# Performance work log

Measured on AMD Instinct MI355X. Metric: run time of the kernel, lower is better.

Reference implementation:

```python
import jax, jax.numpy as jnp
import numpy as np

D_MODEL = 256
D_STATE = 64
D_CONV = 4
EXPAND = 2
HEADDIM = 16
D_INNER = EXPAND * D_MODEL            # 512
NHEADS = D_INNER // HEADDIM           # 32
CONV_DIM = D_INNER + 2 * D_STATE      # 640 (ngroups=1)
D_IN_PROJ = 2 * D_INNER + 2 * D_STATE + NHEADS  # 1184
BATCH = 256
SEQ = 200


def _ln(x, g, b, eps=1e-12):
    m = jnp.mean(x, axis=-1, keepdims=True)
    v = jnp.mean((x - m) ** 2, axis=-1, keepdims=True)
    return (x - m) * jax.lax.rsqrt(v + eps) * g + b


def setup_inputs() -> dict:
    key = jax.random.key(0)
    ks = jax.random.split(key, 16)
    def gn(i, shape, s=0.02):
        return jax.random.normal(ks[i], shape, jnp.float32) * s
    return {
        "input_tensor": jax.random.normal(ks[0], (BATCH, SEQ, D_MODEL), jnp.float32),
        # Mamba2 params
        "in_proj_w": gn(1, (D_MODEL, D_IN_PROJ)),
        "conv_w": gn(2, (CONV_DIM, D_CONV), 0.1),
        "conv_b": jnp.zeros((CONV_DIM,), jnp.float32),
        "dt_bias": gn(3, (NHEADS,), 0.1),
        "A_log": jnp.log(jax.random.uniform(ks[4], (NHEADS,), jnp.float32, 1.0, 16.0)),
        "D_skip": jnp.ones((NHEADS,), jnp.float32),
        "rms_w": jnp.ones((D_INNER,), jnp.float32),
        "out_proj_w": gn(5, (D_INNER, D_MODEL)),
        # Layer norms / mixers
        "ln_g": jnp.ones((D_MODEL,), jnp.float32),
        "ln_b": jnp.zeros((D_MODEL,), jnp.float32),
        "filt_w": gn(6, (1, SEQ // 2 + 1, D_MODEL, 2), 0.02),
        "filt_ln_g": jnp.ones((D_MODEL,), jnp.float32),
        "filt_ln_b": jnp.zeros((D_MODEL,), jnp.float32),
        "alpha": jax.random.uniform(ks[7], (D_MODEL,), jnp.float32),
        "beta": jax.random.uniform(ks[8], (D_MODEL,), jnp.float32),
        # FFN
        "ffn_w1": gn(9, (D_MODEL, 4 * D_MODEL)),
        "ffn_b1": jnp.zeros((4 * D_MODEL,), jnp.float32),
        "ffn_w2": gn(10, (4 * D_MODEL, D_MODEL)),
        "ffn_b2": jnp.zeros((D_MODEL,), jnp.float32),
        "ffn_ln_g": jnp.ones((D_MODEL,), jnp.float32),
        "ffn_ln_b": jnp.zeros((D_MODEL,), jnp.float32),
    }


def _mamba2(x, in_proj_w, conv_w, conv_b, dt_bias, A_log, D_skip, rms_w, out_proj_w):
    b, l, _ = x.shape
    zxbcdt = x @ in_proj_w                                  # [b,l,1184]
    z, xBC, dt = jnp.split(zxbcdt, [D_INNER, D_INNER + CONV_DIM], axis=-1)
    # depthwise causal conv over time + SiLU
    xp = jnp.pad(xBC, ((0, 0), (D_CONV - 1, 0), (0, 0)))
    conv = conv_b + sum(conv_w[:, k] * xp[:, k:k + l, :] for k in range(D_CONV))
    xBC = jax.nn.silu(conv)
    xs, Bm, Cm = jnp.split(xBC, [D_INNER, D_INNER + D_STATE], axis=-1)
    xh = xs.reshape(b, l, NHEADS, HEADDIM)
    dt = jax.nn.softplus(dt + dt_bias)                      # [b,l,h]
    A = -jnp.exp(A_log)                                     # [h]
    dA = jnp.exp(dt * A)                                    # [b,l,h]
    dtx = dt[..., None] * xh                                # [b,l,h,p]

    def step(state, inp):
        dA_t, dtx_t, B_t, C_t = inp
        # state: [b,h,p,n]
        state = dA_t[:, :, None, None] * state + dtx_t[..., None] * B_t[:, None, None, :]
        y_t = jnp.einsum('bhpn,bn->bhp', state, C_t)
        return state, y_t

    state0 = jnp.zeros((b, NHEADS, HEADDIM, D_STATE), x.dtype)
    _, y = jax.lax.scan(step, state0,
                        (jnp.moveaxis(dA, 1, 0), jnp.moveaxis(dtx, 1, 0),
                         jnp.moveaxis(Bm, 1, 0), jnp.moveaxis(Cm, 1, 0)))
    y = jnp.moveaxis(y, 0, 1) + D_skip[None, None, :, None] * xh   # skip connection
    y = y.reshape(b, l, D_INNER)
    # gated RMSNorm: rmsnorm(y * silu(z)) * w
    g = y * jax.nn.silu(z)
    g = g * jax.lax.rsqrt(jnp.mean(g * g, axis=-1, keepdims=True) + 1e-5) * rms_w
    return g @ out_proj_w


def reference(input_tensor, in_proj_w, conv_w, conv_b, dt_bias, A_log, D_skip,
              rms_w, out_proj_w, ln_g, ln_b, filt_w, filt_ln_g, filt_ln_b,
              alpha, beta, ffn_w1, ffn_b1, ffn_w2, ffn_b2, ffn_ln_g, ffn_ln_b):
    x = input_tensor
    h1 = _mamba2(x, in_proj_w, conv_w, conv_b, dt_bias, A_log, D_skip, rms_w, out_proj_w)
    h1 = _ln(h1 + x, ln_g, ln_b)
    # FFT filter branch
    xf = jnp.fft.rfft(x, axis=1, norm='ortho')
    w = filt_w[..., 0] + 1j * filt_w[..., 1]                # [1,101,d]
    xi = jnp.fft.irfft(xf * w, n=SEQ, axis=1, norm='ortho').astype(x.dtype)
    h2 = _ln(xi + x, filt_ln_g, filt_ln_b)
    h = alpha * h1 + beta * h2
    hid = jax.nn.gelu(h @ ffn_w1 + ffn_b1, approximate=False) @ ffn_w2 + ffn_b2
    return _ln(hid + h, ffn_ln_g, ffn_ln_b)
```

## Files before the change

kernel.cpp:

```cpp
#include <hip/hip_runtime.h>
#include <math.h>

#define BATCHN 256
#define SEQ 200
#define DMODEL 256
#define DINNER 512
#define NH 32
#define HD 16
#define DSTATE 64
#define DINPROJ 1184
#define XBCLD 672
#define BL (BATCHN*SEQ)
#define NF 101
#define XBASE 655360
#define TC 20
#define NCH 10
#define XIOFF 8500000

typedef __attribute__((ext_vector_type(8))) short bf16x8;
typedef __attribute__((ext_vector_type(4))) float f32x4;

__device__ inline unsigned short f2bf(float f) {
    union { float f; unsigned u; } v; v.f = f;
    unsigned r = v.u + 0x7FFFu + ((v.u >> 16) & 1u);
    return (unsigned short)(r >> 16);
}
__device__ inline float bf2f(unsigned short h) {
    union { unsigned u; float f; } v; v.u = ((unsigned)h) << 16;
    return v.f;
}

#define GLOAD16(src, dst) __builtin_amdgcn_global_load_lds( \
    (const __attribute__((address_space(1))) void*)(src),   \
    (__attribute__((address_space(3))) void*)(dst), 16, 0, 0)

__global__ void init_dft_kernel(unsigned short* __restrict__ EF, unsigned short* __restrict__ EI)
{
    const float ang = 6.28318530717958647692f / 200.0f;
    int idx = blockIdx.x * 256 + threadIdx.x;
    if (idx < 256 * SEQ) {
        int f = idx / SEQ, t = idx - f * SEQ;
        float v;
        if (f <= 100) { int ph = (f * t) % 200; v = cosf(ang * (float)ph); }
        else if (f <= 201) { int ff = f - 101; int ph = (ff * t) % 200; v = -sinf(ang * (float)ph); }
        else v = 0.f;
        EF[idx] = f2bf(v);
    } else if (idx < 256 * SEQ + 256 * 256) {
        int j2 = idx - 256 * SEQ;
        int t = j2 >> 8, j = j2 & 255;
        float v;
        if (t >= 200) v = 0.f;
        else if (j == 0) v = 1.0f / 200.0f;
        else if (j == 100) v = ((t & 1) ? -1.0f : 1.0f) / 200.0f;
        else if (j < 100) { int ph = (j * t) % 200; v = 2.0f * cosf(ang * (float)ph) / 200.0f; }
        else if (j >= 202 || j == 101 || j == 201) v = 0.0f;
        else { int f = j - 101; int ph = (f * t) % 200; v = -2.0f * sinf(ang * (float)ph) / 200.0f; }
        EI[j2] = f2bf(v);
    }
}

#define S0 303104
#define S1 131072
#define S2 262144
#define S3 262144
#define S4 1638400
__global__ void setup_kernel(const float* __restrict__ ipw, const float* __restrict__ opw,
                             const float* __restrict__ w1, const float* __restrict__ w2,
                             const float* __restrict__ X,
                             unsigned short* __restrict__ wTall, unsigned short* __restrict__ opwT,
                             unsigned short* __restrict__ w1T, unsigned short* __restrict__ w2T,
                             unsigned short* __restrict__ xbf)
{
    long long idx = (long long)blockIdx.x * 256 + threadIdx.x;
    if (idx < S0) { int n = (int)(idx / 256), k = (int)(idx % 256);
        wTall[idx] = f2bf(ipw[(long long)k * DINPROJ + n]); return; }
    idx -= S0;
    if (idx < S1) { int n = (int)(idx / 512), k = (int)(idx % 512);
        opwT[idx] = f2bf(opw[(long long)k * 256 + n]); return; }
    idx -= S1;
    if (idx < S2) { int n = (int)(idx / 256), k = (int)(idx % 256);
        w1T[idx] = f2bf(w1[(long long)k * 1024 + n]); return; }
    idx -= S2;
    if (idx < S3) { int n = (int)(idx / 1024), k = (int)(idx % 1024);
        w2T[idx] = f2bf(w2[(long long)k * 256 + n]); return; }
    idx -= S3;
    if (idx < S4) {
        long long i = idx * 8;
        float4 a = ((const float4*)(X + i))[0];
        float4 b = ((const float4*)(X + i))[1];
        uint4 o;
        o.x = (unsigned)f2bf(a.x) | ((unsigned)f2bf(a.y) << 16);
        o.y = (unsigned)f2bf(a.z) | ((unsigned)f2bf(a.w) << 16);
        o.z = (unsigned)f2bf(b.x) | ((unsigned)f2bf(b.y) << 16);
        o.w = (unsigned)f2bf(b.z) | ((unsigned)f2bf(b.w) << 16);
        *(uint4*)(xbf + i) = o;
    }
}

__global__ void xT_kernel(const float* __restrict__ X, unsigned short* __restrict__ XT)
{
    __shared__ float tile[32][33];
    int b = blockIdx.z, t0 = blockIdx.x * 32, d0 = blockIdx.y * 32;
    int tx = threadIdx.x & 31, ty = threadIdx.x >> 5;
    const float* xb = X + (long long)b * SEQ * DMODEL;
#pragma unroll
    for (int i = 0; i < 4; i++) {
        int t = t0 + ty + i * 8;
        tile[ty + i * 8][tx] = (t < SEQ) ? xb[(long long)t * DMODEL + d0 + tx] : 0.f;
    }
    __syncthreads();
    unsigned short* xtb = XT + (long long)b * DMODEL * SEQ;
#pragma unroll
    for (int i = 0; i < 4; i++) {
        int d = d0 + ty + i * 8;
        int t = t0 + tx;
        if (t < SEQ) xtb[(long long)d * SEQ + t] = f2bf(tile[tx][ty + i * 8]);
    }
}

template<int ACT, int CBF>
__global__ __launch_bounds__(256) void mgemm_kernel(
    const unsigned short* __restrict__ Ab, const unsigned short* __restrict__ BTp,
    void* __restrict__ Cp, const float* __restrict__ bias,
    int M, int N, int K, int lda, int ldbt, int ldc,
    long long sA, long long sBT, long long sC)
{
    __shared__ unsigned short As[128 * 32];
    __shared__ unsigned short Bs[128 * 32];
    const unsigned short* Aa = Ab + (long long)blockIdx.z * sA;
    const unsigned short* Bt = BTp + (long long)blockIdx.z * sBT;
    float* Cf = (float*)Cp + (CBF ? 0 : (long long)blockIdx.z * sC);
    unsigned short* Cb = (unsigned short*)Cp + (CBF ? (long long)blockIdx.z * sC : 0);

    int m0 = blockIdx.y * 128, n0 = blockIdx.x * 128;
    int tid = threadIdx.x;
    int srow = tid >> 1, skb = (tid & 1) * 16;
    int w = tid >> 6, l = tid & 63;
    int wr = w >> 1, wc = w & 1;
    int fr = l & 15, fk = l >> 4;
    int glr = (w << 4) + (l >> 2);
    int glc = (l & 3) << 3;
    bool fullM = (m0 + 128 <= M);
    bool fullN = (n0 + 128 <= N);

    f32x4 acc[4][4] = {};

    for (int k0 = 0; k0 < K; k0 += 32) {
        bool kedge = (k0 + 32 > K);
        if (fullM && !kedge) {
            GLOAD16(Aa + (long long)(m0 + glr) * lda + k0 + glc,      &As[w << 9]);
            GLOAD16(Aa + (long long)(m0 + 64 + glr) * lda + k0 + glc, &As[2048 + (w << 9)]);
        } else {
            int gm = m0 + srow;
            unsigned short* dst = &As[srow * 32 + skb];
#pragma unroll
            for (int i = 0; i < 16; i++) {
                int gk = k0 + skb + i;
                dst[i] = (gm < M && gk < K) ? Aa[(long long)gm * lda + gk] : (unsigned short)0;
            }
        }
        if (fullN && !kedge) {
            GLOAD16(Bt + (long long)(n0 + glr) * ldbt + k0 + glc,      &Bs[w << 9]);
            GLOAD16(Bt + (long long)(n0 + 64 + glr) * ldbt + k0 + glc, &Bs[2048 + (w << 9)]);
        } else {
            int gn = n0 + srow;
            unsigned short* dst = &Bs[srow * 32 + skb];
#pragma unroll
            for (int i = 0; i < 16; i++) {
                int gk = k0 + skb + i;
                dst[i] = (gn < N && gk < K) ? Bt[(long long)gn * ldbt + gk] : (unsigned short)0;
            }
        }
        __syncthreads();
        bf16x8 a[4], b[4];
#pragma unroll
        for (int i = 0; i < 4; i++) {
            a[i] = *(const bf16x8*)&As[(wr * 64 + i * 16 + fr) * 32 + fk * 8];
            b[i] = *(const bf16x8*)&Bs[(wc * 64 + i * 16 + fr) * 32 + fk * 8];
        }
#pragma unroll
        for (int i = 0; i < 4; i++)
#pragma unroll
            for (int j = 0; j < 4; j++)
                acc[i][j] = __builtin_amdgcn_mfma_f32_16x16x32_bf16(a[i], b[j], acc[i][j], 0, 0, 0);
        __syncthreads();
    }

#pragma unroll
    for (int i = 0; i < 4; i++) {
        int gr0 = m0 + wr * 64 + i * 16 + fk * 4;
#pragma unroll
        for (int j = 0; j < 4; j++) {
            int gc = n0 + wc * 64 + j * 16 + fr;
            if (gc >= N) continue;
            float bv = bias ? bias[gc] : 0.f;
#pragma unroll
            for (int r = 0; r < 4; r++) {
                int gr = gr0 + r;
                if (gr >= M) continue;
                float v = acc[i][j][r] + bv;
                if (ACT == 1) v = 0.5f * v * (1.f + erff(v * 0.70710678118654752f));
                long long ci = (long long)gr * ldc + gc;
                if (CBF) Cb[ci] = f2bf(v);
                else Cf[ci] = v;
            }
        }
    }
}

__global__ __launch_bounds__(256) void mgemm_proj(
    const unsigned short* __restrict__ Aa, const unsigned short* __restrict__ Bt,
    float* __restrict__ XBCout, unsigned short* __restrict__ Zout)
{
    __shared__ unsigned short As[128 * 32];
    __shared__ unsigned short Bs[128 * 32];
    const int N = DINPROJ;
    int m0 = blockIdx.y * 128, n0 = blockIdx.x * 128;
    int tid = threadIdx.x;
    int srow = tid >> 1, skb = (tid & 1) * 16;
    int w = tid >> 6, l = tid & 63;
    int wr = w >> 1, wc = w & 1;
    int fr = l & 15, fk = l >> 4;
    int glr = (w << 4) + (l >> 2);
    int glc = (l & 3) << 3;
    bool fullN = (n0 + 128 <= N);

    f32x4 acc[4][4] = {};

    for (int k0 = 0; k0 < 256; k0 += 32) {
        GLOAD16(Aa + (long long)(m0 + glr) * 256 + k0 + glc,      &As[w << 9]);
        GLOAD16(Aa + (long long)(m0 + 64 + glr) * 256 + k0 + glc, &As[2048 + (w << 9)]);
        if (fullN) {
            GLOAD16(Bt + (long long)(n0 + glr) * 256 + k0 + glc,      &Bs[w << 9]);
            GLOAD16(Bt + (long long)(n0 + 64 + glr) * 256 + k0 + glc, &Bs[2048 + (w << 9)]);
        } else {
            int gn = n0 + srow;
            unsigned short* dst = &Bs[srow * 32 + skb];
#pragma unroll
            for (int i = 0; i < 16; i++)
                dst[i] = (gn < N) ? Bt[(long long)gn * 256 + k0 + skb + i] : (unsigned short)0;
        }
        __syncthreads();
        bf16x8 a[4], b[4];
#pragma unroll
        for (int i = 0; i < 4; i++) {
            a[i] = *(const bf16x8*)&As[(wr * 64 + i * 16 + fr) * 32 + fk * 8];
            b[i] = *(const bf16x8*)&Bs[(wc * 64 + i * 16 + fr) * 32 + fk * 8];
        }
#pragma unroll
        for (int i = 0; i < 4; i++)
#pragma unroll
            for (int j = 0; j < 4; j++)
                acc[i][j] = __builtin_amdgcn_mfma_f32_16x16x32_bf16(a[i], b[j], acc[i][j], 0, 0, 0);
        __syncthreads();
    }

#pragma unroll
    for (int i = 0; i < 4; i++) {
        int gr0 = m0 + wr * 64 + i * 16 + fk * 4;
#pragma unroll
        for (int j = 0; j < 4; j++) {
            int gc = n0 + wc * 64 + j * 16 + fr;
            if (gc >= N) continue;
#pragma unroll
            for (int r = 0; r < 4; r++) {
                int gr = gr0 + r;
                float v = acc[i][j][r];
                if (gc < 512) Zout[(long long)gr * 512 + gc] = f2bf(v);
                else XBCout[(long long)gr * XBCLD + (gc - 512)] = v;
            }
        }
    }
}

__global__ void convbc_kernel(const float* __restrict__ XBC, const float* __restrict__ conv_w,
                              const float* __restrict__ conv_b, const float* __restrict__ dt_bias,
                              const float* __restrict__ A_log,
                              float* __restrict__ BCb, float* __restrict__ DTb, float* __restrict__ DAb,
                              float* __restrict__ BCF)
{
    __shared__ float sB[64];
    int row = blockIdx.x;
    int b = row / SEQ, l = row - b * SEQ;
    int tid = threadIdx.x;
    float v = 0.f;
    if (tid < 128) {
        int ch = 512 + tid;
        float acc = conv_b[ch];
#pragma unroll
        for (int k = 0; k < 4; k++) {
            int lt = l + k - 3;
            if (lt >= 0)
                acc = fmaf(conv_w[ch * 4 + k], XBC[(long long)(b * SEQ + lt) * XBCLD + ch], acc);
        }
        v = acc * __builtin_amdgcn_rcpf(1.f + __expf(-acc));
        BCb[(long long)row * 128 + tid] = v;
        if (tid < 64) sB[tid] = v;
    } else if (tid < 160) {
        int h = tid - 128;
        float draw = XBC[(long long)row * XBCLD + 640 + h] + dt_bias[h];
        float dtv = (draw > 20.f) ? draw : log1pf(__expf(draw));
        DTb[(long long)row * NH + h] = dtv;
        DAb[(long long)row * NH + h] = __expf(-__expf(A_log[h]) * dtv);
    }
    __syncthreads();
    if (tid >= 64 && tid < 128) {
        int n = tid - 64;
        float prod = sB[n] * v;
#pragma unroll
        for (int m = 1; m < 64; m <<= 1) prod += __shfl_xor(prod, m);
        if (n == 0) BCF[row] = prod;
    }
}

__device__ __forceinline__ void sstep2(
    float raw, float dtv, float da, float bc,
    const float4& qb0, const float4& qb1, const float4& qb2, const float4& qb3,
    const float4& qc0, const float4& qc1, const float4& qc2, const float4& qc3,
    float cw0, float cw1, float cw2, float cw3, float cb, float ds,
    float* st, float& w0, float& w1, float& w2,
    int lane, float* __restrict__ yaddr)
{
    float cvv = cb + cw0 * w0 + cw1 * w1 + cw2 * w2 + cw3 * raw;
    float xhv = cvv * __builtin_amdgcn_rcpf(1.f + __expf(-cvv));
    w0 = w1; w1 = w2; w2 = raw;
    float xv = dtv * xhv;
    float p0 = st[0]  * qc0.x;
    float p1 = st[1]  * qc0.y;
    float p2 = st[2]  * qc0.z;
    float p3 = st[3]  * qc0.w;
    p0 = fmaf(st[4],  qc1.x, p0);
    p1 = fmaf(st[5],  qc1.y, p1);
    p2 = fmaf(st[6],  qc1.z, p2);
    p3 = fmaf(st[7],  qc1.w, p3);
    p0 = fmaf(st[8],  qc2.x, p0);
    p1 = fmaf(st[9],  qc2.y, p1);
    p2 = fmaf(st[10], qc2.z, p2);
    p3 = fmaf(st[11], qc2.w, p3);
    p0 = fmaf(st[12], qc3.x, p0);
    p1 = fmaf(st[13], qc3.y, p1);
    p2 = fmaf(st[14], qc3.z, p2);
    p3 = fmaf(st[15], qc3.w, p3);
    st[0]  = fmaf(da, st[0],  xv * qb0.x);
    st[1]  = fmaf(da, st[1],  xv * qb0.y);
    st[2]  = fmaf(da, st[2],  xv * qb0.z);
    st[3]  = fmaf(da, st[3],  xv * qb0.w);
    st[4]  = fmaf(da, st[4],  xv * qb1.x);
    st[5]  = fmaf(da, st[5],  xv * qb1.y);
    st[6]  = fmaf(da, st[6],  xv * qb1.z);
    st[7]  = fmaf(da, st[7],  xv * qb1.w);
    st[8]  = fmaf(da, st[8],  xv * qb2.x);
    st[9]  = fmaf(da, st[9],  xv * qb2.y);
    st[10] = fmaf(da, st[10], xv * qb2.z);
    st[11] = fmaf(da, st[11], xv * qb2.w);
    st[12] = fmaf(da, st[12], xv * qb3.x);
    st[13] = fmaf(da, st[13], xv * qb3.y);
    st[14] = fmaf(da, st[14], xv * qb3.z);
    st[15] = fmaf(da, st[15], xv * qb3.w);
    float part = (p0 + p1) + (p2 + p3);
    part += __shfl_xor(part, 16);
    part += __shfl_xor(part, 32);
    if (lane < HD) *yaddr = fmaf(da, part, fmaf(xv, bc, ds * xhv));
}

__global__ __launch_bounds__(256) void scan7b_kernel(
    const float* __restrict__ DTb, const float* __restrict__ DAb,
    float* __restrict__ XBC, const float* __restrict__ BCb,
    const float* __restrict__ Dsk,
    const float* __restrict__ conv_w, const float* __restrict__ conv_b,
    const float* __restrict__ BCF)
{
    __shared__ float sbc[2][TC][128];
    __shared__ unsigned short sx[2][TC][128];
    __shared__ float sdt[2][TC][8];
    __shared__ float sda[2][TC][8];
    __shared__ float sbcf[2][TC];
    int tid = threadIdx.x;
    int wv = tid >> 6, lane = tid & 63;
    int bid = blockIdx.x;
    int b = bid >> 2, hq = (bid & 3) * 8;
    long long rowb = (long long)b * SEQ;

    for (int i = tid; i < TC * 32; i += 256) {
        int r = i >> 5, c = i & 31;
        ((float4*)&sbc[0][r][0])[c] = ((const float4*)(BCb + (rowb + r) * 128))[c];
    }
    for (int i = tid; i < TC * 64; i += 256) {
        int r = i >> 6, c2 = i & 63;
        float2 v = *(const float2*)(XBC + (rowb + r) * XBCLD + hq * 16 + (c2 << 1));
        *(unsigned*)&sx[0][r][c2 << 1] = (unsigned)f2bf(v.x) | ((unsigned)f2bf(v.y) << 16);
    }
    for (int i = tid; i < TC * 8; i += 256) {
        int t = i >> 3, j = i & 7;
        sdt[0][t][j] = DTb[(rowb + t) * NH + hq + j];
        sda[0][t][j] = DAb[(rowb + t) * NH + hq + j];
    }
    if (tid < TC) sbcf[0][tid] = BCF[rowb + tid];
    __syncthreads();

    int p = lane & 15, g = lane >> 4;
    int hA = hq + wv, hB = hq + 4 + wv;
    int chA = hA * HD + p, chB = hB * HD + p;
    float cwA0 = conv_w[chA * 4 + 0], cwA1 = conv_w[chA * 4 + 1];
    float cwA2 = conv_w[chA * 4 + 2], cwA3 = conv_w[chA * 4 + 3];
    float cbA = conv_b[chA];
    float cwB0 = conv_w[chB * 4 + 0], cwB1 = conv_w[chB * 4 + 1];
    float cwB2 = conv_w[chB * 4 + 2], cwB3 = conv_w[chB * 4 + 3];
    float cbB = conv_b[chB];
    float dsA = Dsk[hA], dsB = Dsk[hB];
    int xcA = wv * 16 + p, xcB = (4 + wv) * 16 + p;
    float* ypA = XBC + rowb * XBCLD + hA * HD + p;
    float* ypB = XBC + rowb * XBCLD + hB * HD + p;
    float stA[16], stB[16];
#pragma unroll
    for (int r = 0; r < 16; r++) { stA[r] = 0.f; stB[r] = 0.f; }
    float wA0 = 0.f, wA1 = 0.f, wA2 = 0.f;
    float wB0 = 0.f, wB1 = 0.f, wB2 = 0.f;

    for (int c = 0; c < NCH; c++) {
        int cur = c & 1;
        if (c + 1 < NCH) {
            int nb = cur ^ 1;
            long long tb = rowb + (c + 1) * TC;
            for (int i = tid; i < TC * 32; i += 256) {
                int r = i >> 5, cc = i & 31;
                ((float4*)&sbc[nb][r][0])[cc] = ((const float4*)(BCb + (tb + r) * 128))[cc];
            }
            for (int i = tid; i < TC * 64; i += 256) {
                int r = i >> 6, c2 = i & 63;
                float2 v = *(const float2*)(XBC + (tb + r) * XBCLD + hq * 16 + (c2 << 1));
                *(unsigned*)&sx[nb][r][c2 << 1] = (unsigned)f2bf(v.x) | ((unsigned)f2bf(v.y) << 16);
            }
            for (int i = tid; i < TC * 8; i += 256) {
                int t = i >> 3, j = i & 7;
                sdt[nb][t][j] = DTb[(tb + t) * NH + hq + j];
                sda[nb][t][j] = DAb[(tb + t) * NH + hq + j];
            }
            if (tid < TC) sbcf[nb][tid] = BCF[tb + tid];
        }
        int tbase = c * TC;
        for (int t = 0; t < TC; t++) {
            int gt = tbase + t;
            const float4* qb = (const float4*)&sbc[cur][t][g * 16];
            const float4* qc = (const float4*)&sbc[cur][t][64 + g * 16];
            float4 qb0 = qb[0], qb1 = qb[1], qb2 = qb[2], qb3 = qb[3];
            float4 qc0 = qc[0], qc1 = qc[1], qc2 = qc[2], qc3 = qc[3];
            float rawA = bf2f(sx[cur][t][xcA]);
            float rawB = bf2f(sx[cur][t][xcB]);
            float bc = sbcf[cur][t];
            sstep2(rawA, sdt[cur][t][wv], sda[cur][t][wv], bc,
                   qb0, qb1, qb2, qb3, qc0, qc1, qc2, qc3,
                   cwA0, cwA1, cwA2, cwA3, cbA, dsA, stA, wA0, wA1, wA2,
                   lane, ypA + (long long)gt * XBCLD);
            sstep2(rawB, sdt[cur][t][4 + wv], sda[cur][t][4 + wv], bc,
                   qb0, qb1, qb2, qb3, qc0, qc1, qc2, qc3,
                   cwB0, cwB1, cwB2, cwB3, cbB, dsB, stB, wB0, wB1, wB2,
                   lane, ypB + (long long)gt * XBCLD);
        }
        __syncthreads();
    }
}

__global__ __launch_bounds__(256) void gate_kernel(
    float* __restrict__ XBC, const unsigned short* __restrict__ Zbf,
    const float* __restrict__ rms_w)
{
    int row = blockIdx.x * 4 + (threadIdx.x >> 6);
    int lane = threadIdx.x & 63;
    float* yrow = XBC + (long long)row * XBCLD + lane * 8;
    const unsigned short* zrow = Zbf + (long long)row * 512 + lane * 8;
    float4 y0 = ((const float4*)yrow)[0];
    float4 y1 = ((const float4*)yrow)[1];
    uint4 zq = ((const uint4*)zrow)[0];
    float yv[8] = { y0.x, y0.y, y0.z, y0.w, y1.x, y1.y, y1.z, y1.w };
    float zv[8];
    zv[0] = bf2f((unsigned short)(zq.x & 0xFFFF)); zv[1] = bf2f((unsigned short)(zq.x >> 16));
    zv[2] = bf2f((unsigned short)(zq.y & 0xFFFF)); zv[3] = bf2f((unsigned short)(zq.y >> 16));
    zv[4] = bf2f((unsigned short)(zq.z & 0xFFFF)); zv[5] = bf2f((unsigned short)(zq.z >> 16));
    zv[6] = bf2f((unsigned short)(zq.w & 0xFFFF)); zv[7] = bf2f((unsigned short)(zq.w >> 16));
    float a[8]; float ss = 0.f;
#pragma unroll
    for (int i = 0; i < 8; i++) {
        float z = zv[i];
        a[i] = yv[i] * (z * __builtin_amdgcn_rcpf(1.f + __expf(-z)));
        ss = fmaf(a[i], a[i], ss);
    }
#pragma unroll
    for (int m = 1; m < 64; m <<= 1) ss += __shfl_xor(ss, m);
    float sc = rsqrtf(ss * (1.f / 512.f) + 1e-5f);
    const float* rw = rms_w + lane * 8;
    float4 r0 = ((const float4*)rw)[0];
    float4 r1 = ((const float4*)rw)[1];
    float rv[8] = { r0.x, r0.y, r0.z, r0.w, r1.x, r1.y, r1.z, r1.w };
    uint4 o;
    o.x = (unsigned)f2bf(a[0] * sc * rv[0]) | ((unsigned)f2bf(a[1] * sc * rv[1]) << 16);
    o.y = (unsigned)f2bf(a[2] * sc * rv[2]) | ((unsigned)f2bf(a[3] * sc * rv[3]) << 16);
    o.z = (unsigned)f2bf(a[4] * sc * rv[4]) | ((unsigned)f2bf(a[5] * sc * rv[5]) << 16);
    o.w = (unsigned)f2bf(a[6] * sc * rv[6]) | ((unsigned)f2bf(a[7] * sc * rv[7]) << 16);
    unsigned short* grow = (unsigned short*)(XBC + (long long)row * XBCLD);
    ((uint4*)grow)[lane] = o;
}

__global__ void lnadd_bf_kernel(const unsigned short* __restrict__ A, const float* __restrict__ Bb,
                                const float* __restrict__ g, const float* __restrict__ be,
                                float* __restrict__ O)
{
    int row = blockIdx.x * 4 + (threadIdx.x >> 6);
    int lane = threadIdx.x & 63;
    long long base = (long long)row * DMODEL + lane * 4;
    float v[4]; float s1 = 0.f;
#pragma unroll
    for (int i = 0; i < 4; i++) { float a = bf2f(A[base + i]) + Bb[base + i]; v[i] = a; s1 += a; }
#pragma unroll
    for (int m = 1; m < 64; m <<= 1) s1 += __shfl_xor(s1, m);
    float mean = s1 * (1.f / 256.f);
    float s2 = 0.f;
#pragma unroll
    for (int i = 0; i < 4; i++) { float d = v[i] - mean; s2 = fmaf(d, d, s2); }
#pragma unroll
    for (int m = 1; m < 64; m <<= 1) s2 += __shfl_xor(s2, m);
    float r = rsqrtf(s2 * (1.f / 256.f) + 1e-12f);
#pragma unroll
    for (int i = 0; i < 4; i++)
        O[base + i] = (v[i] - mean) * r * g[lane * 4 + i] + be[lane * 4 + i];
}

__global__ void combine2_kernel(const float* __restrict__ XI, const float* __restrict__ X,
                                float* __restrict__ MO, unsigned short* __restrict__ HB,
                                const float* __restrict__ lg, const float* __restrict__ lb,
                                const float* __restrict__ fg, const float* __restrict__ fb,
                                const float* __restrict__ al, const float* __restrict__ bt)
{
    int row = blockIdx.x * 4 + (threadIdx.x >> 6);
    int lane = threadIdx.x & 63;
    long long base = (long long)row * DMODEL + lane * 4;
    int bb = row / SEQ, ll = row - bb * SEQ;
    long long xib = (long long)bb * 65536 + ll * 256 + lane * 4;
    float u[4], v[4]; float su = 0.f, sv = 0.f;
#pragma unroll
    for (int i = 0; i < 4; i++) {
        float xv = X[base + i];
        float a = MO[base + i] + xv;
        float b = XI[xib + i] + xv;
        u[i] = a; v[i] = b; su += a; sv += b;
    }
#pragma unroll
    for (int m = 1; m < 64; m <<= 1) { su += __shfl_xor(su, m); sv += __shfl_xor(sv, m); }
    float mu = su * (1.f / 256.f), mv = sv * (1.f / 256.f);
    float qu = 0.f, qv = 0.f;
#pragma unroll
    for (int i = 0; i < 4; i++) {
        float du = u[i] - mu; qu = fmaf(du, du, qu);
        float dv = v[i] - mv; qv = fmaf(dv, dv, qv);
    }
#pragma unroll
    for (int m = 1; m < 64; m <<= 1) { qu += __shfl_xor(qu, m); qv += __shfl_xor(qv, m); }
    float ru = rsqrtf(qu * (1.f / 256.f) + 1e-12f);
    float rv = rsqrtf(qv * (1.f / 256.f) + 1e-12f);
#pragma unroll
    for (int i = 0; i < 4; i++) {
        int d = lane * 4 + i;
        float h1 = (u[i] - mu) * ru * lg[d] + lb[d];
        float h2 = (v[i] - mv) * rv * fg[d] + fb[d];
        float h = al[d] * h1 + bt[d] * h2;
        MO[base + i] = h;
        HB[base + i] = f2bf(h);
    }
}

__global__ void filt_kernel(unsigned short* __restrict__ XF, const float* __restrict__ W)
{
    long long idx = (long long)blockIdx.x * 256 + threadIdx.x;
    if (idx >= (long long)BATCHN * DMODEL * NF) return;
    int f = (int)(idx % NF);
    int d = (int)((idx / NF) % DMODEL);
    int b = (int)(idx / ((long long)NF * DMODEL));
    long long base = ((long long)b * DMODEL + d) * 256;
    float re = bf2f(XF[base + f]);
    float im = bf2f(XF[base + 101 + f]);
    float wr = W[((long long)f * DMODEL + d) * 2];
    float wi = W[((long long)f * DMODEL + d) * 2 + 1];
    XF[base + f]       = f2bf(re * wr - im * wi);
    XF[base + 101 + f] = f2bf(re * wi + im * wr);
}

extern "C" void kernel_launch(void* const* d_in, const int* in_sizes, int n_in,
                              void* d_out, int out_size, void* d_ws, size_t ws_size,
                              hipStream_t stream)
{
    const float* x          = (const float*)d_in[0];
    const float* in_proj_w  = (const float*)d_in[1];
    const float* conv_w     = (const float*)d_in[2];
    const float* conv_b     = (const float*)d_in[3];
    const float* dt_bias    = (const float*)d_in[4];
    const float* A_log      = (const float*)d_in[5];
    const float* D_skip     = (const float*)d_in[6];
    const float* rms_w      = (const float*)d_in[7];
    const float* out_proj_w = (const float*)d_in[8];
    const float* ln_g       = (const float*)d_in[9];
    const float* ln_b       = (const float*)d_in[10];
    const float* filt_w     = (const float*)d_in[11];
    const float* filt_ln_g  = (const float*)d_in[12];
    const float* filt_ln_b  = (const float*)d_in[13];
    const float* alpha      = (const float*)d_in[14];
    const float* beta       = (const float*)d_in[15];
    const float* ffn_w1     = (const float*)d_in[16];
    const float* ffn_b1     = (const float*)d_in[17];
    const float* ffn_w2     = (const float*)d_in[18];
    const float* ffn_b2     = (const float*)d_in[19];
    const float* ffn_ln_g   = (const float*)d_in[20];
    const float* ffn_ln_b   = (const float*)d_in[21];
    float* out = (float*)d_out;
    float* ws = (float*)d_ws;

    unsigned short* WP    = (unsigned short*)(ws + 81920);
    unsigned short* wTall = WP;
    unsigned short* opwT  = wTall + 1184 * 256;
    unsigned short* w1T   = opwT + 256 * 512;
    unsigned short* w2T   = w1T + 1024 * 256;
    unsigned short* EFbf  = w2T + 256 * 1024;
    unsigned short* EIbf  = EFbf + 256 * SEQ;
    float* XBC = ws + XBASE;
    float* BCb = XBC + (long long)BL * XBCLD;
    float* DTb = BCb + (long long)BL * 128;
    float* DAb = DTb + (long long)BL * NH;
    float* MO  = DAb + (long long)BL * NH;
    float* BCF = MO + (long long)BL * DMODEL;
    unsigned short* Zbf = (unsigned short*)MO;
    unsigned short* xbf  = (unsigned short*)BCb;
    unsigned short* xTbf = (unsigned short*)BCb;
    unsigned short* MObf = (unsigned short*)BCb;
    unsigned short* Gbf = (unsigned short*)XBC;
    unsigned short* XFT = (unsigned short*)XBC;
    float* XI  = XBC + XIOFF;
    unsigned short* HID = (unsigned short*)XBC;
    unsigned short* FFO = (unsigned short*)(XBC + 26500000);

    init_dft_kernel<<<dim3((256 * SEQ + 256 * 256 + 255) / 256), dim3(256), 0, stream>>>(EFbf, EIbf);
    setup_kernel<<<dim3((S0 + S1 + S2 + S3 + S4) / 256), dim3(256), 0, stream>>>(
        in_proj_w, out_proj_w, ffn_w1, ffn_w2, x, wTall, opwT, w1T, w2T, xbf);

    mgemm_proj<<<dim3(10, BL / 128), dim3(256), 0, stream>>>(xbf, wTall, XBC, Zbf);

    convbc_kernel<<<dim3(BL), dim3(192), 0, stream>>>(XBC, conv_w, conv_b, dt_bias, A_log,
                                                      BCb, DTb, DAb, BCF);

    scan7b_kernel<<<dim3(BATCHN * 4), dim3(256), 0, stream>>>(DTb, DAb, XBC, BCb, D_skip,
                                                              conv_w, conv_b, BCF);

    xT_kernel<<<dim3(7, 8, BATCHN), dim3(256), 0, stream>>>(x, xTbf);

    gate_kernel<<<dim3(BL / 4), dim3(256), 0, stream>>>(XBC, Zbf, rms_w);

    mgemm_kernel<0,0><<<dim3(2, BL / 128, 1), dim3(256), 0, stream>>>(
        Gbf, opwT, MO, nullptr, BL, 256, 512, 1344, 512, 256, 0, 0, 0);

    mgemm_kernel<0,1><<<dim3(2, 2, BATCHN), dim3(256), 0, stream>>>(
        xTbf, EFbf, XFT, nullptr, 256, 256, SEQ, SEQ, SEQ, 256,
        (long long)DMODEL * SEQ, 0, 65536);

    filt_kernel<<<dim3((BATCHN * DMODEL * NF + 255) / 256), dim3(256), 0, stream>>>(XFT, filt_w);

    mgemm_kernel<0,0><<<dim3(2, 2, BATCHN), dim3(256), 0, stream>>>(
        EIbf, XFT, XI, nullptr, 256, 256, 256, 256, 256, 256,
        0, 65536, 65536);

    combine2_kernel<<<dim3(BL / 4), dim3(256), 0, stream>>>(XI, x, MO, MObf,
                                                            ln_g, ln_b, filt_ln_g, filt_ln_b,
                                                            alpha, beta);

    mgemm_kernel<1,1><<<dim3(8, BL / 128, 1), dim3(256), 0, stream>>>(
        MObf, w1T, HID, ffn_b1, BL, 1024, 256, 256, 256, 1024, 0, 0, 0);

    mgemm_kernel<0,1><<<dim3(2, BL / 128, 1), dim3(256), 0, stream>>>(
        HID, w2T, FFO, ffn_b2, BL, 256, 1024, 1024, 1024, 256, 0, 0, 0);

    lnadd_bf_kernel<<<dim3(BL / 4), dim3(256), 0, stream>>>(FFO, MO, ffn_ln_g, ffn_ln_b, out);
}
```

Measured before the change: 814.2 us.

## Tile conv/BC kernel over 25-step chunks and drop fp32 residual write

Replaces the one-row-per-block conv/B/C kernel with a kernel that loads a 28-row window of B/C channels into shared memory once per 25-timestep chunk, so each input row is read from global memory about once instead of four times and far fewer blocks are launched. The combine kernel no longer writes the fp32 mixed activation; the final layernorm reads the bf16 copy instead. This cuts global traffic, but the final residual add now runs at bf16 precision, which may change numerics slightly.

```diff
diff --git a/kernel.cpp b/kernel.cpp
--- a/kernel.cpp
+++ b/kernel.cpp
@@ -273,43 +273,54 @@
     }
 }
 
-__global__ void convbc_kernel(const float* __restrict__ XBC, const float* __restrict__ conv_w,
-                              const float* __restrict__ conv_b, const float* __restrict__ dt_bias,
-                              const float* __restrict__ A_log,
-                              float* __restrict__ BCb, float* __restrict__ DTb, float* __restrict__ DAb,
-                              float* __restrict__ BCF)
-{
-    __shared__ float sB[64];
-    int row = blockIdx.x;
-    int b = row / SEQ, l = row - b * SEQ;
+__global__ __launch_bounds__(256) void convbc2_kernel(
+    const float* __restrict__ XBC, const float* __restrict__ conv_w,
+    const float* __restrict__ conv_b, const float* __restrict__ dt_bias,
+    const float* __restrict__ A_log,
+    float* __restrict__ BCb, float* __restrict__ DTb, float* __restrict__ DAb,
+    float* __restrict__ BCF)
+{
+    __shared__ float swin[28][128];
+    __shared__ float sv[25][128];
     int tid = threadIdx.x;
-    float v = 0.f;
-    if (tid < 128) {
-        int ch = 512 + tid;
-        float acc = conv_b[ch];
-#pragma unroll
-        for (int k = 0; k < 4; k++) {
-            int lt = l + k - 3;
-            if (lt >= 0)
-                acc = fmaf(conv_w[ch * 4 + k], XBC[(long long)(b * SEQ + lt) * XBCLD + ch], acc);
-        }
-        v = acc * __builtin_amdgcn_rcpf(1.f + __expf(-acc));
-        BCb[(long long)row * 128 + tid] = v;
-        if (tid < 64) sB[tid] = v;
-    } else if (tid < 160) {
-        int h = tid - 128;
-        float draw = XBC[(long long)row * XBCLD + 640 + h] + dt_bias[h];
+    int bid = blockIdx.x;
+    int b = bid >> 3, c = bid & 7;
+    int t0 = c * 25;
+    long long rowb = (long long)b * SEQ;
+    for (int i = tid; i < 28 * 32; i += 256) {
+        int r = i >> 5, q = i & 31;
+        int t = t0 - 3 + r;
+        float4 v = (t >= 0) ? ((const float4*)(XBC + (rowb + t) * XBCLD + 512))[q]
+                            : (float4){0.f, 0.f, 0.f, 0.f};
+        ((float4*)&swin[r][0])[q] = v;
+    }
+    for (int i = tid; i < 25 * 32; i += 256) {
+        int r = i >> 5, h = i & 31;
+        long long row = rowb + t0 + r;
+        float draw = XBC[row * XBCLD + 640 + h] + dt_bias[h];
         float dtv = (draw > 20.f) ? draw : log1pf(__expf(draw));
-        DTb[(long long)row * NH + h] = dtv;
-        DAb[(long long)row * NH + h] = __expf(-__expf(A_log[h]) * dtv);
+        DTb[row * NH + h] = dtv;
+        DAb[row * NH + h] = __expf(-__expf(A_log[h]) * dtv);
     }
     __syncthreads();
-    if (tid >= 64 && tid < 128) {
-        int n = tid - 64;
-        float prod = sB[n] * v;
+    for (int i = tid; i < 25 * 128; i += 256) {
+        int r = i >> 7, ch = i & 127;
+        int gch = 512 + ch;
+        float acc = conv_b[gch];
+#pragma unroll
+        for (int k = 0; k < 4; k++)
+            acc = fmaf(conv_w[gch * 4 + k], swin[r + k][ch], acc);
+        float v = acc * __builtin_amdgcn_rcpf(1.f + __expf(-acc));
+        BCb[(rowb + t0 + r) * 128 + ch] = v;
+        sv[r][ch] = v;
+    }
+    __syncthreads();
+    int wv = tid >> 6, lane = tid & 63;
+    for (int r = wv; r < 25; r += 4) {
+        float prod = sv[r][lane] * sv[r][64 + lane];
 #pragma unroll
         for (int m = 1; m < 64; m <<= 1) prod += __shfl_xor(prod, m);
-        if (n == 0) BCF[row] = prod;
+        if (lane == 0) BCF[rowb + t0 + r] = prod;
     }
 }
 
@@ -501,7 +512,7 @@
     ((uint4*)grow)[lane] = o;
 }
 
-__global__ void lnadd_bf_kernel(const unsigned short* __restrict__ A, const float* __restrict__ Bb,
+__global__ void lnadd_bb_kernel(const unsigned short* __restrict__ A, const unsigned short* __restrict__ Bb,
                                 const float* __restrict__ g, const float* __restrict__ be,
                                 float* __restrict__ O)
 {
@@ -510,7 +521,7 @@
     long long base = (long long)row * DMODEL + lane * 4;
     float v[4]; float s1 = 0.f;
 #pragma unroll
-    for (int i = 0; i < 4; i++) { float a = bf2f(A[base + i]) + Bb[base + i]; v[i] = a; s1 += a; }
+    for (int i = 0; i < 4; i++) { float a = bf2f(A[base + i]) + bf2f(Bb[base + i]); v[i] = a; s1 += a; }
 #pragma unroll
     for (int m = 1; m < 64; m <<= 1) s1 += __shfl_xor(s1, m);
     float mean = s1 * (1.f / 256.f);
@@ -526,7 +537,7 @@
 }
 
 __global__ void combine2_kernel(const float* __restrict__ XI, const float* __restrict__ X,
-                                float* __restrict__ MO, unsigned short* __restrict__ HB,
+                                const float* __restrict__ MO, unsigned short* __restrict__ HB,
                                 const float* __restrict__ lg, const float* __restrict__ lb,
                                 const float* __restrict__ fg, const float* __restrict__ fb,
                                 const float* __restrict__ al, const float* __restrict__ bt)
@@ -563,7 +574,6 @@
         float h1 = (u[i] - mu) * ru * lg[d] + lb[d];
         float h2 = (v[i] - mv) * rv * fg[d] + fb[d];
         float h = al[d] * h1 + bt[d] * h2;
-        MO[base + i] = h;
         HB[base + i] = f2bf(h);
     }
 }
@@ -642,8 +652,8 @@
 
     mgemm_proj<<<dim3(10, BL / 128), dim3(256), 0, stream>>>(xbf, wTall, XBC, Zbf);
 
-    convbc_kernel<<<dim3(BL), dim3(192), 0, stream>>>(XBC, conv_w, conv_b, dt_bias, A_log,
-                                                      BCb, DTb, DAb, BCF);
+    convbc2_kernel<<<dim3(BATCHN * 8), dim3(256), 0, stream>>>(XBC, conv_w, conv_b, dt_bias,
+                                                               A_log, BCb, DTb, DAb, BCF);
 
     scan7b_kernel<<<dim3(BATCHN * 4), dim3(256), 0, stream>>>(DTb, DAb, XBC, BCb, D_skip,
                                                               conv_w, conv_b, BCF);
@@ -675,5 +685,5 @@
     mgemm_kernel<0,1><<<dim3(2, BL / 128, 1), dim3(256), 0, stream>>>(
         HID, w2T, FFO, ffn_b2, BL, 256, 1024, 1024, 1024, 256, 0, 0, 0);
 
-    lnadd_bf_kernel<<<dim3(BL / 4), dim3(256), 0, stream>>>(FFO, MO, ffn_ln_g, ffn_ln_b, out);
-}
+    lnadd_bb_kernel<<<dim3(BL / 4), dim3(256), 0, stream>>>(FFO, MObf, ffn_ln_g, ffn_ln_b, out);
+}
```

New measurement: 790.5 us. 2.9% less time.
